# Kernel optimization log

Hardware: AMD Instinct MI355X
Metric: run time of the kernel (lower is better)

The kernel has to match this reference:

```python
import jax, jax.numpy as jnp
import numpy as np

NDIV = (10, 10)
OUT_CHANNEL = 100


def setup_inputs() -> dict:
    key = jax.random.key(0)
    k1, k2 = jax.random.split(key)
    x1 = jax.random.normal(k1, (8, 64, 128, 128), dtype=jnp.float32)
    x2 = jax.random.normal(k2, (8, 64, 60, 60), dtype=jnp.float32)
    return {"x1": x1, "x2": x2}


def reference(x1, x2):
    B, C, H, W = x1.shape
    h, w = x2.shape[-2], x2.shape[-1]
    nd0, nd1 = NDIV
    hh, ww = h // nd0, w // nd1  # patch size (6, 6)
    P = nd0 * nd1                # 100 patches per sample

    # channel-wise L2 normalization (dim=1)
    x1n = x1 / jnp.linalg.norm(x1, axis=1, keepdims=True)
    x2n = x2 / jnp.linalg.norm(x2, axis=1, keepdims=True)

    # extract nd0*nd1 patches per sample as conv filters: [B*P, C, hh, ww]
    patches = x2n.reshape(B, C, nd0, hh, nd1, ww)
    patches = patches.transpose(0, 2, 4, 1, 3, 5).reshape(B * P, C, hh, ww)

    # grouped cross-correlation (torch F.conv2d = correlation, no kernel flip)
    lhs = x1n.reshape(1, B * C, H, W)
    mm = jax.lax.conv_general_dilated(
        lhs, patches,
        window_strides=(1, 1),
        padding=((hh // 2, hh // 2), (ww // 2, ww // 2)),
        feature_group_count=B,
        dimension_numbers=("NCHW", "OIHW", "NCHW"),
    ) / (hh * ww)  # [1, B*P, H+1, W+1] for even hh,ww

    # bilinear resize to (H, W)  (torch align_corners=False == half-pixel)
    mm = jax.image.resize(mm, (1, B * P, H, W), method="bilinear")

    # [B, P, H, W] -> topk over patch dim, then mean
    mm = mm.reshape(B, P, H, W)
    topv = jax.lax.top_k(jnp.moveaxis(mm, 1, -1), OUT_CHANNEL)[0]  # [B,H,W,k]
    out = jnp.mean(topv, axis=-1)[:, None]  # [B,1,H,W]
    return out
```

## Files before the change

kernel.cpp:

```cpp
#include <hip/hip_runtime.h>
#include <cstddef>

#define BB   8
#define CC   64
#define H1   128
#define W1   128
#define HW1  (H1*W1)
#define HS   60
#define WS   60
#define HO   129
#define WO   129

#define G     16
#define CPG   4
#define HR    38
#define HC    75
#define HSTR  76
#define NST   12
#define PSTR  132
#define PPLANE (HO*PSTR)

__global__ __launch_bounds__(256) void k_inv1(const float* __restrict__ x1,
                                              float* __restrict__ inv1) {
    int idx = blockIdx.x * 256 + threadIdx.x;
    int b  = idx >> 14;
    int hw = idx & 16383;
    const float* p = x1 + (size_t)b * CC * HW1 + hw;
    float s = 0.f;
#pragma unroll
    for (int c = 0; c < CC; ++c) {
        float v = p[c * HW1];
        s += v * v;
    }
    inv1[idx] = 1.0f / sqrtf(s);
}

__global__ __launch_bounds__(256) void k_inv2(const float* __restrict__ x2,
                                              float* __restrict__ inv2) {
    __shared__ float red[256];
    int tid = threadIdx.x;
    int pix = blockIdx.x * 64 + (tid & 63);
    int csub = tid >> 6;
    int b  = pix / (HS * WS);
    int hw = pix % (HS * WS);
    const float* p = x2 + ((size_t)b * CC + csub * 16) * (HS * WS) + hw;
    float s = 0.f;
#pragma unroll
    for (int c = 0; c < 16; ++c) {
        float v = p[c * (HS * WS)];
        s += v * v;
    }
    red[tid] = s;
    __syncthreads();
    if (tid < 64) {
        float t = red[tid] + red[tid + 64] + red[tid + 128] + red[tid + 192];
        inv2[blockIdx.x * 64 + tid] = 1.0f / sqrtf(t);
    }
}

__global__ __launch_bounds__(256) void k_fold(const float* __restrict__ x2,
                                              const float* __restrict__ inv2,
                                              float* __restrict__ S) {
    __shared__ float bins[36];
    int tid = threadIdx.x;
    int bc  = blockIdx.x;
    int b   = bc >> 6;
    if (tid < 36) bins[tid] = 0.f;
    __syncthreads();
    const float* px = x2 + (size_t)bc * (HS * WS);
    const float* pn = inv2 + b * (HS * WS);
    for (int i = tid; i < HS * WS; i += 256) {
        int hh = i / WS, ww = i - hh * WS;
        int bin = (hh % 6) * 6 + (ww % 6);
        atomicAdd(&bins[bin], px[i] * pn[i]);
    }
    __syncthreads();
    if (tid < 36) S[bc * 36 + tid] = bins[tid];
}

__global__ __launch_bounds__(256) void k_conv(const float* __restrict__ x1,
                                              const float* __restrict__ inv1,
                                              const float* __restrict__ S,
                                              float* __restrict__ part) {
    int blk = blockIdx.x;
    int xt = blk & 1;
    int yt = (blk >> 1) & 3;
    int b  = (blk >> 3) & 7;
    int g  = blk >> 6;
    int x0 = xt * 64, y0 = yt * 32;
    int tid = threadIdx.x;
    int txq = tid & 15, ty = tid >> 4;

    __shared__ float buf[2][HR * HSTR];

    const float* x1b   = x1 + (size_t)b * CC * HW1;
    const float* inv1b = inv1 + b * HW1;

    int   goff[NST];
    float vinv[NST];
    int   lofs[NST];
#pragma unroll
    for (int k = 0; k < NST; ++k) {
        int i = tid + 256 * k;
        int r  = i / HC;
        int cl = i - r * HC;
        int gy = y0 - 3 + r, gx = x0 - 3 + cl;
        bool v = (i < HR * HC) && gy >= 0 && gy < H1 && gx >= 0 && gx < W1;
        goff[k] = v ? gy * W1 + gx : 0;
        vinv[k] = v ? inv1b[gy * W1 + gx] : 0.0f;
        lofs[k] = (i < HR * HC) ? r * HSTR + cl : 0;
    }

    float acc0[5] = {0,0,0,0,0};
    float acc1[5] = {0,0,0,0,0};
    float acc2[5] = {0,0,0,0,0};
    const bool doR2 = (ty == 15) && (y0 == 96);
    const bool c5   = (x0 == 64) && (txq == 15);

    int ch0 = g * CPG;
    const float* Sb = S + ((size_t)b * CC + ch0) * 36;

    float a[NST];
#pragma unroll
    for (int k = 0; k < NST; ++k)
        a[k] = x1b[(size_t)ch0 * HW1 + goff[k]] * vinv[k];

    for (int ci = 0; ci < CPG; ++ci) {
        float* bp = buf[ci & 1];
#pragma unroll
        for (int k = 0; k < NST; ++k) {
            if (k < 11) bp[lofs[k]] = a[k];
            else if (tid < (HR * HC - 11 * 256)) bp[lofs[k]] = a[k];
        }
        __syncthreads();

        if (ci + 1 < CPG) {
#pragma unroll
            for (int k = 0; k < NST; ++k)
                a[k] = x1b[(size_t)(ch0 + ci + 1) * HW1 + goff[k]] * vinv[k];
        }

        const float* Sc = Sb + ci * 36;
        float sv[36];
#pragma unroll
        for (int t = 0; t < 36; ++t) sv[t] = Sc[t];

        const float* base = bp + 4 * txq;
#pragma unroll
        for (int rr = 0; rr < 7; ++rr) {
            int row = 2 * ty + rr;
            const float4* rp = (const float4*)(base + row * HSTR);
            float4 q0 = rp[0], q1 = rp[1], q2 = rp[2];
            float r[12] = {q0.x,q0.y,q0.z,q0.w, q1.x,q1.y,q1.z,q1.w,
                           q2.x,q2.y,q2.z,q2.w};
            if (rr <= 5) {
#pragma unroll
                for (int j = 0; j < 5; ++j)
#pragma unroll
                    for (int dx = 0; dx < 6; ++dx)
                        acc0[j] += r[j + dx] * sv[rr * 6 + dx];
            }
            if (rr >= 1) {
#pragma unroll
                for (int j = 0; j < 5; ++j)
#pragma unroll
                    for (int dx = 0; dx < 6; ++dx)
                        acc1[j] += r[j + dx] * sv[(rr - 1) * 6 + dx];
            }
            if (doR2 && rr >= 2) {
#pragma unroll
                for (int j = 0; j < 5; ++j)
#pragma unroll
                    for (int dx = 0; dx < 6; ++dx)
                        acc2[j] += r[j + dx] * sv[(rr - 2) * 6 + dx];
            }
        }
        if (doR2) {
            int row = 2 * ty + 7;
            const float4* rp = (const float4*)(base + row * HSTR);
            float4 q0 = rp[0], q1 = rp[1], q2 = rp[2];
            float r[12] = {q0.x,q0.y,q0.z,q0.w, q1.x,q1.y,q1.z,q1.w,
                           q2.x,q2.y,q2.z,q2.w};
#pragma unroll
            for (int j = 0; j < 5; ++j)
#pragma unroll
                for (int dx = 0; dx < 6; ++dx)
                    acc2[j] += r[j + dx] * sv[5 * 6 + dx];
        }
    }

    float* pb = part + ((size_t)g * BB + b) * PPLANE;
    int orow = y0 + 2 * ty;
    int ocol = x0 + 4 * txq;
    *(float4*)(pb + (size_t)orow * PSTR + ocol) =
        make_float4(acc0[0], acc0[1], acc0[2], acc0[3]);
    *(float4*)(pb + (size_t)(orow + 1) * PSTR + ocol) =
        make_float4(acc1[0], acc1[1], acc1[2], acc1[3]);
    if (c5) {
        pb[(size_t)orow * PSTR + 128] = acc0[4];
        pb[(size_t)(orow + 1) * PSTR + 128] = acc1[4];
    }
    if (doR2) {
        *(float4*)(pb + (size_t)128 * PSTR + ocol) =
            make_float4(acc2[0], acc2[1], acc2[2], acc2[3]);
        if (c5) pb[(size_t)128 * PSTR + 128] = acc2[4];
    }
}

__global__ __launch_bounds__(256) void k_reduce(const float* __restrict__ part,
                                                float* __restrict__ out129) {
    int idx = blockIdx.x * 256 + threadIdx.x;
    if (idx >= BB * HO * WO) return;
    int b = idx / (HO * WO);
    int p = idx % (HO * WO);
    int row = p / WO, col = p - row * WO;
    float s = 0.f;
#pragma unroll
    for (int g = 0; g < G; ++g)
        s += part[((size_t)g * BB + b) * PPLANE + (size_t)row * PSTR + col];
    out129[idx] = s * (1.0f / 3600.0f);
}

__global__ __launch_bounds__(256) void k_resize(const float* __restrict__ out129,
                                                float* __restrict__ out) {
    int idx = blockIdx.x * 256 + threadIdx.x;
    int b  = idx >> 14;
    int oy = (idx >> 7) & 127;
    int ox = idx & 127;

    const float inv_scale = 129.0f / 128.0f;
    const float ksc       = 128.0f / 129.0f;

    float sy = (oy + 0.5f) * inv_scale - 0.5f;
    float sx = (ox + 0.5f) * inv_scale - 0.5f;
    int fy = (int)floorf(sy);
    int fx = (int)floorf(sx);

    float wy[4], wx[4];
    float sumy = 0.f, sumx = 0.f;
#pragma unroll
    for (int k = 0; k < 4; ++k) {
        int jy = fy - 1 + k;
        float w = 0.f;
        if (jy >= 0 && jy < HO) w = fmaxf(0.f, 1.0f - fabsf(sy - (float)jy) * ksc);
        wy[k] = w; sumy += w;
        int jx = fx - 1 + k;
        float w2 = 0.f;
        if (jx >= 0 && jx < WO) w2 = fmaxf(0.f, 1.0f - fabsf(sx - (float)jx) * ksc);
        wx[k] = w2; sumx += w2;
    }

    const float* p = out129 + (size_t)b * (HO * WO);
    float r = 0.f;
#pragma unroll
    for (int ky = 0; ky < 4; ++ky) {
        if (wy[ky] == 0.f) continue;
        int jy = fy - 1 + ky;
        float rowv = 0.f;
#pragma unroll
        for (int kx = 0; kx < 4; ++kx) {
            if (wx[kx] == 0.f) continue;
            rowv += wx[kx] * p[jy * WO + (fx - 1 + kx)];
        }
        r += wy[ky] * rowv;
    }
    out[idx] = r / (sumy * sumx);
}

extern "C" void kernel_launch(void* const* d_in, const int* in_sizes, int n_in,
                              void* d_out, int out_size, void* d_ws, size_t ws_size,
                              hipStream_t stream) {
    const float* x1 = (const float*)d_in[0];
    const float* x2 = (const float*)d_in[1];
    float* out = (float*)d_out;

    float* ws     = (float*)d_ws;
    float* inv1   = ws;
    float* inv2   = inv1 + BB * HW1;
    float* Sbuf   = inv2 + BB * HS * WS;
    float* part   = Sbuf + BB * CC * 36;
    float* out129 = part + (size_t)G * BB * PPLANE;

    k_inv1  <<<(BB * HW1) / 256, 256, 0, stream>>>(x1, inv1);
    k_inv2  <<<(BB * HS * WS) / 64, 256, 0, stream>>>(x2, inv2);
    k_fold  <<<BB * CC, 256, 0, stream>>>(x2, inv2, Sbuf);
    k_conv  <<<2 * 4 * BB * G, 256, 0, stream>>>(x1, inv1, Sbuf, part);
    k_reduce<<<(BB * HO * WO + 255) / 256, 256, 0, stream>>>(part, out129);
    k_resize<<<(BB * HW1) / 256, 256, 0, stream>>>(out129, out);
}
```

Baseline: 134.9 us.

## Pre-normalize padded x1 and stream conv tiles via async global-to-LDS loads

Replaces the inverse-norm kernel with one that writes a fully normalized, zero-padded copy of x1 (144x134 per plane). The conv kernel then copies each tile straight into LDS with global_load_lds, with no per-element scaling or bounds checks, double-buffered across channels. It also switches to 64x64 output tiles with 4 rows per thread so each LDS row is reused more. The cost is an extra write and re-read of a padded x1 copy (about 39 MB) and half as many conv blocks.

```diff
diff --git a/kernel.cpp b/kernel.cpp
--- a/kernel.cpp
+++ b/kernel.cpp
@@ -11,28 +11,46 @@
 #define HO   129
 #define WO   129
 
+#define PWD  144
+#define PHT  134
+#define PPL  (PHT*PWD)
+
 #define G     16
 #define CPG   4
-#define HR    38
-#define HC    75
-#define HSTR  76
-#define NST   12
+#define T4    19
+#define TROWS 70
+#define NSLOT (TROWS*T4)
 #define PSTR  132
 #define PPLANE (HO*PSTR)
 
-__global__ __launch_bounds__(256) void k_inv1(const float* __restrict__ x1,
-                                              float* __restrict__ inv1) {
+typedef unsigned int u32;
+__device__ __forceinline__ void async_g2l(const float* g, float4* l) {
+    __builtin_amdgcn_global_load_lds((const __attribute__((address_space(1))) u32*)g,
+                                     (__attribute__((address_space(3))) u32*)l,
+                                     16, 0, 0);
+}
+
+__global__ __launch_bounds__(256) void k_norm1(const float* __restrict__ x1,
+                                               float* __restrict__ x1n) {
     int idx = blockIdx.x * 256 + threadIdx.x;
-    int b  = idx >> 14;
-    int hw = idx & 16383;
-    const float* p = x1 + (size_t)b * CC * HW1 + hw;
-    float s = 0.f;
-#pragma unroll
-    for (int c = 0; c < CC; ++c) {
-        float v = p[c * HW1];
-        s += v * v;
-    }
-    inv1[idx] = 1.0f / sqrtf(s);
+    int b  = idx / PPL;
+    int pp = idx - b * PPL;
+    int pr = pp / PWD, pc = pp - pr * PWD;
+    int gy = pr - 3, gx = pc - 3;
+    float* outp = x1n + (size_t)b * CC * PPL + pp;
+    if ((unsigned)gy < 128u && (unsigned)gx < 128u) {
+        const float* p = x1 + (size_t)b * CC * HW1 + gy * W1 + gx;
+        float v[CC];
+        float s = 0.f;
+#pragma unroll
+        for (int c = 0; c < CC; ++c) { v[c] = p[c * HW1]; s += v[c] * v[c]; }
+        float inv = 1.0f / sqrtf(s);
+#pragma unroll
+        for (int c = 0; c < CC; ++c) outp[c * PPL] = v[c] * inv;
+    } else {
+#pragma unroll
+        for (int c = 0; c < CC; ++c) outp[c * PPL] = 0.f;
+    }
 }
 
 __global__ __launch_bounds__(256) void k_inv2(const float* __restrict__ x2,
@@ -78,132 +96,136 @@
     if (tid < 36) S[bc * 36 + tid] = bins[tid];
 }
 
-__global__ __launch_bounds__(256) void k_conv(const float* __restrict__ x1,
-                                              const float* __restrict__ inv1,
+__global__ __launch_bounds__(256) void k_conv(const float* __restrict__ x1n,
                                               const float* __restrict__ S,
                                               float* __restrict__ part) {
     int blk = blockIdx.x;
-    int xt = blk & 1;
-    int yt = (blk >> 1) & 3;
-    int b  = (blk >> 3) & 7;
-    int g  = blk >> 6;
-    int x0 = xt * 64, y0 = yt * 32;
+    int x0 = (blk & 1) * 64;
+    int y0 = ((blk >> 1) & 1) * 64;
+    int b  = (blk >> 2) & 7;
+    int g  = blk >> 5;
     int tid = threadIdx.x;
-    int txq = tid & 15, ty = tid >> 4;
-
-    __shared__ float buf[2][HR * HSTR];
-
-    const float* x1b   = x1 + (size_t)b * CC * HW1;
-    const float* inv1b = inv1 + b * HW1;
-
-    int   goff[NST];
-    float vinv[NST];
-    int   lofs[NST];
-#pragma unroll
-    for (int k = 0; k < NST; ++k) {
+    int tx = tid & 15, ty = tid >> 4;
+    int wv = tid >> 6;
+
+    __shared__ float4 lbuf[2][NSLOT];
+    __shared__ float4 svf[CPG][9];
+
+    if (tid < CPG * 36)
+        ((float*)svf)[tid] = S[((size_t)b * CC + g * CPG) * 36 + tid];
+
+    int off[6];
+#pragma unroll
+    for (int k = 0; k < 6; ++k) {
         int i = tid + 256 * k;
-        int r  = i / HC;
-        int cl = i - r * HC;
-        int gy = y0 - 3 + r, gx = x0 - 3 + cl;
-        bool v = (i < HR * HC) && gy >= 0 && gy < H1 && gx >= 0 && gx < W1;
-        goff[k] = v ? gy * W1 + gx : 0;
-        vinv[k] = v ? inv1b[gy * W1 + gx] : 0.0f;
-        lofs[k] = (i < HR * HC) ? r * HSTR + cl : 0;
-    }
-
-    float acc0[5] = {0,0,0,0,0};
-    float acc1[5] = {0,0,0,0,0};
-    float acc2[5] = {0,0,0,0,0};
-    const bool doR2 = (ty == 15) && (y0 == 96);
-    const bool c5   = (x0 == 64) && (txq == 15);
-
-    int ch0 = g * CPG;
-    const float* Sb = S + ((size_t)b * CC + ch0) * 36;
-
-    float a[NST];
-#pragma unroll
-    for (int k = 0; k < NST; ++k)
-        a[k] = x1b[(size_t)ch0 * HW1 + goff[k]] * vinv[k];
+        int r = i / T4, c4 = i - r * T4;
+        off[k] = (y0 + r) * PWD + x0 + 4 * c4;
+    }
+
+    const float* gbase = x1n + ((size_t)b * CC + g * CPG) * PPL;
+
+#pragma unroll
+    for (int k = 0; k < 5; ++k)
+        async_g2l(gbase + off[k], &lbuf[0][wv * 64 + 256 * k]);
+    if (tid < NSLOT - 1280)
+        async_g2l(gbase + off[5], &lbuf[0][wv * 64 + 1280]);
+
+    float acc[4][5] = {{0,0,0,0,0},{0,0,0,0,0},{0,0,0,0,0},{0,0,0,0,0}};
+    float accE[5] = {0,0,0,0,0};
+    const bool doC4 = (x0 == 64) && (tx == 15);
+    const bool doR4 = (y0 == 64) && (ty == 15);
 
     for (int ci = 0; ci < CPG; ++ci) {
-        float* bp = buf[ci & 1];
-#pragma unroll
-        for (int k = 0; k < NST; ++k) {
-            if (k < 11) bp[lofs[k]] = a[k];
-            else if (tid < (HR * HC - 11 * 256)) bp[lofs[k]] = a[k];
-        }
         __syncthreads();
 
         if (ci + 1 < CPG) {
-#pragma unroll
-            for (int k = 0; k < NST; ++k)
-                a[k] = x1b[(size_t)(ch0 + ci + 1) * HW1 + goff[k]] * vinv[k];
-        }
-
-        const float* Sc = Sb + ci * 36;
-        float sv[36];
-#pragma unroll
-        for (int t = 0; t < 36; ++t) sv[t] = Sc[t];
-
-        const float* base = bp + 4 * txq;
-#pragma unroll
-        for (int rr = 0; rr < 7; ++rr) {
-            int row = 2 * ty + rr;
-            const float4* rp = (const float4*)(base + row * HSTR);
+            const float* gp = gbase + (size_t)(ci + 1) * PPL;
+            float4* dst = lbuf[(ci + 1) & 1];
+#pragma unroll
+            for (int k = 0; k < 5; ++k)
+                async_g2l(gp + off[k], &dst[wv * 64 + 256 * k]);
+            if (tid < NSLOT - 1280)
+                async_g2l(gp + off[5], &dst[wv * 64 + 1280]);
+        }
+
+        float s[36];
+        const float4* sp = (const float4*)svf[ci];
+#pragma unroll
+        for (int t = 0; t < 9; ++t) {
+            float4 w = sp[t];
+            s[4*t] = w.x; s[4*t+1] = w.y; s[4*t+2] = w.z; s[4*t+3] = w.w;
+        }
+
+        const float4* tb = lbuf[ci & 1];
+#pragma unroll
+        for (int rr = 0; rr < 9; ++rr) {
+            const float4* rp = tb + (4 * ty + rr) * T4 + tx;
             float4 q0 = rp[0], q1 = rp[1], q2 = rp[2];
             float r[12] = {q0.x,q0.y,q0.z,q0.w, q1.x,q1.y,q1.z,q1.w,
                            q2.x,q2.y,q2.z,q2.w};
-            if (rr <= 5) {
-#pragma unroll
-                for (int j = 0; j < 5; ++j)
+#pragma unroll
+            for (int q = 0; q < 4; ++q) {
+                int dy = rr - q;
+                if (dy >= 0 && dy < 6) {
+#pragma unroll
+                    for (int j = 0; j < 4; ++j)
+#pragma unroll
+                        for (int dx = 0; dx < 6; ++dx)
+                            acc[q][j] += r[j + dx] * s[dy * 6 + dx];
+                    if (doC4) {
+#pragma unroll
+                        for (int dx = 0; dx < 6; ++dx)
+                            acc[q][4] += r[4 + dx] * s[dy * 6 + dx];
+                    }
+                }
+            }
+            if (doR4 && rr >= 4) {
+                int dy = rr - 4;
+#pragma unroll
+                for (int j = 0; j < 4; ++j)
 #pragma unroll
                     for (int dx = 0; dx < 6; ++dx)
-                        acc0[j] += r[j + dx] * sv[rr * 6 + dx];
+                        accE[j] += r[j + dx] * s[dy * 6 + dx];
+                if (doC4) {
+#pragma unroll
+                    for (int dx = 0; dx < 6; ++dx)
+                        accE[4] += r[4 + dx] * s[dy * 6 + dx];
+                }
             }
-            if (rr >= 1) {
-#pragma unroll
-                for (int j = 0; j < 5; ++j)
-#pragma unroll
-                    for (int dx = 0; dx < 6; ++dx)
-                        acc1[j] += r[j + dx] * sv[(rr - 1) * 6 + dx];
-            }
-            if (doR2 && rr >= 2) {
-#pragma unroll
-                for (int j = 0; j < 5; ++j)
-#pragma unroll
-                    for (int dx = 0; dx < 6; ++dx)
-                        acc2[j] += r[j + dx] * sv[(rr - 2) * 6 + dx];
-            }
-        }
-        if (doR2) {
-            int row = 2 * ty + 7;
-            const float4* rp = (const float4*)(base + row * HSTR);
+        }
+        if (doR4) {
+            const float4* rp = tb + (4 * ty + 9) * T4 + tx;
             float4 q0 = rp[0], q1 = rp[1], q2 = rp[2];
             float r[12] = {q0.x,q0.y,q0.z,q0.w, q1.x,q1.y,q1.z,q1.w,
                            q2.x,q2.y,q2.z,q2.w};
 #pragma unroll
-            for (int j = 0; j < 5; ++j)
+            for (int j = 0; j < 4; ++j)
 #pragma unroll
                 for (int dx = 0; dx < 6; ++dx)
-                    acc2[j] += r[j + dx] * sv[5 * 6 + dx];
+                    accE[j] += r[j + dx] * s[30 + dx];
+            if (doC4) {
+#pragma unroll
+                for (int dx = 0; dx < 6; ++dx)
+                    accE[4] += r[4 + dx] * s[30 + dx];
+            }
         }
     }
 
     float* pb = part + ((size_t)g * BB + b) * PPLANE;
-    int orow = y0 + 2 * ty;
-    int ocol = x0 + 4 * txq;
-    *(float4*)(pb + (size_t)orow * PSTR + ocol) =
-        make_float4(acc0[0], acc0[1], acc0[2], acc0[3]);
-    *(float4*)(pb + (size_t)(orow + 1) * PSTR + ocol) =
-        make_float4(acc1[0], acc1[1], acc1[2], acc1[3]);
-    if (c5) {
-        pb[(size_t)orow * PSTR + 128] = acc0[4];
-        pb[(size_t)(orow + 1) * PSTR + 128] = acc1[4];
-    }
-    if (doR2) {
+    int orow = y0 + 4 * ty, ocol = x0 + 4 * tx;
+#pragma unroll
+    for (int q = 0; q < 4; ++q)
+        *(float4*)(pb + (size_t)(orow + q) * PSTR + ocol) =
+            make_float4(acc[q][0], acc[q][1], acc[q][2], acc[q][3]);
+    if (doC4) {
+#pragma unroll
+        for (int q = 0; q < 4; ++q)
+            pb[(size_t)(orow + q) * PSTR + 128] = acc[q][4];
+    }
+    if (doR4) {
         *(float4*)(pb + (size_t)128 * PSTR + ocol) =
-            make_float4(acc2[0], acc2[1], acc2[2], acc2[3]);
-        if (c5) pb[(size_t)128 * PSTR + 128] = acc2[4];
+            make_float4(accE[0], accE[1], accE[2], accE[3]);
+        if (doC4) pb[(size_t)128 * PSTR + 128] = accE[4];
     }
 }
 
@@ -275,16 +297,16 @@
     float* out = (float*)d_out;
 
     float* ws     = (float*)d_ws;
-    float* inv1   = ws;
-    float* inv2   = inv1 + BB * HW1;
+    float* inv2   = ws;
     float* Sbuf   = inv2 + BB * HS * WS;
-    float* part   = Sbuf + BB * CC * 36;
+    float* x1n    = Sbuf + BB * CC * 36;
+    float* part   = x1n + (size_t)BB * CC * PPL;
     float* out129 = part + (size_t)G * BB * PPLANE;
 
-    k_inv1  <<<(BB * HW1) / 256, 256, 0, stream>>>(x1, inv1);
+    k_norm1 <<<(BB * PPL) / 256, 256, 0, stream>>>(x1, x1n);
     k_inv2  <<<(BB * HS * WS) / 64, 256, 0, stream>>>(x2, inv2);
     k_fold  <<<BB * CC, 256, 0, stream>>>(x2, inv2, Sbuf);
-    k_conv  <<<2 * 4 * BB * G, 256, 0, stream>>>(x1, inv1, Sbuf, part);
+    k_conv  <<<4 * BB * G, 256, 0, stream>>>(x1n, Sbuf, part);
     k_reduce<<<(BB * HO * WO + 255) / 256, 256, 0, stream>>>(part, out129);
     k_resize<<<(BB * HW1) / 256, 256, 0, stream>>>(out129, out);
 }
```

After: 140.6 us. +4.3%, slower.
